# Kernel optimization log

Measured on AMD Instinct MI355X. Metric: run time of the kernel, lower is better.

Reference implementation:

```python
import jax, jax.numpy as jnp
import numpy as np

B, TV, TE = 128, 32, 64
VOCAB, EMB, H, REPR, NET, MAXLEN = 1024, 256, 512, 128, 8, 32


def setup_inputs() -> dict:
    key = jax.random.key(0)
    ks = jax.random.split(key, 26)
    g = lambda i, shape: jax.random.normal(ks[i], shape, dtype=jnp.float32) * 0.05
    return dict(
        input_vertex=jax.random.randint(ks[0], (B, TV), 0, VOCAB),
        input_edge=jax.random.randint(ks[1], (B, TE, 3), 0, NET),
        vertex_emb=g(2, (VOCAB, EMB)),
        v_Wi=g(3, (3 * H, EMB)), v_Wh=g(4, (3 * H, H)), v_bi=g(5, (3 * H,)), v_bh=g(6, (3 * H,)),
        vout_W=g(7, (VOCAB, H)), vout_b=g(8, (VOCAB,)),
        vrep_W=g(9, (REPR, H)), vrep_b=g(10, (REPR,)),
        edge_emb=g(11, (MAXLEN, EMB)),
        e_Wi=g(12, (3 * H, 2 * EMB)), e_Wh=g(13, (3 * H, H)), e_bi=g(14, (3 * H,)), e_bh=g(15, (3 * H,)),
        erep_W=g(16, (REPR, H)), erep_b=g(17, (REPR,)),
        etype_W=g(18, (NET, REPR)), etype_b=g(19, (NET,)),
        src_w=g(20, (REPR,)), src_b=g(21, ()),
        dst_w=g(22, (REPR,)), dst_b=g(23, ()),
    )


def _gru_scan(X, Wi, Wh, bi, bh):
    # X: [T, B, D] -> hidden states [T, B, H]; torch GRUCell gate order r,z,n
    gi = jnp.einsum('tbd,gd->tbg', X, Wi) + bi  # precompute input projections
    h0 = jnp.zeros((X.shape[1], Wh.shape[1]), X.dtype)

    def step(h, gi_t):
        gh = h @ Wh.T + bh
        ir, iz, inn = jnp.split(gi_t, 3, axis=-1)
        hr, hz, hn = jnp.split(gh, 3, axis=-1)
        r = jax.nn.sigmoid(ir + hr)
        z = jax.nn.sigmoid(iz + hz)
        n = jnp.tanh(inn + r * hn)
        h_new = (1.0 - z) * n + z * h
        return h_new, h_new

    _, hs = jax.lax.scan(step, h0, gi)
    return hs


def reference(input_vertex, input_edge, vertex_emb, v_Wi, v_Wh, v_bi, v_bh,
              vout_W, vout_b, vrep_W, vrep_b, edge_emb, e_Wi, e_Wh, e_bi, e_bh,
              erep_W, erep_b, etype_W, etype_b, src_w, src_b, dst_w, dst_b):
    # ---- vertex RNN ----
    Ve = vertex_emb[input_vertex].transpose(1, 0, 2)          # [Tv, B, emb]
    hv = _gru_scan(Ve, v_Wi, v_Wh, v_bi, v_bh)                # [Tv, B, H]
    O_vertex = jnp.einsum('tbh,vh->bvt', hv, vout_W) + vout_b[None, :, None]  # [B, vocab, Tv]
    vrep = jnp.einsum('tbh,rh->tbr', hv, vrep_W) + vrep_b     # [Tv, B, repr]

    # ---- edge RNN ----
    E = jnp.concatenate([edge_emb[input_edge[:, :, 0]],
                         edge_emb[input_edge[:, :, 1]]], axis=2)  # [B, Te, 2*emb]
    he = _gru_scan(E.transpose(1, 0, 2), e_Wi, e_Wh, e_bi, e_bh)  # [Te, B, H]
    e = jnp.einsum('tbh,rh->tbr', he, erep_W) + erep_b            # [Te, B, repr]
    O_edge_type = jnp.einsum('ebr,kr->bke', e, etype_W) + etype_b[None, :, None]  # [B, n_et, Te]

    # ---- edge-vertex additive attention: tanh(e + v) ----
    u = jnp.tanh(e[:, None] + vrep[None])                     # [Te, Tv, B, repr]
    osrc = jnp.einsum('evbr,r->bve', u, src_w) + src_b        # [B, Tv, Te]
    odst = jnp.einsum('evbr,r->bve', u, dst_w) + dst_b        # [B, Tv, Te]
    O_edge = jnp.stack([osrc, odst], axis=2)                  # [B, Tv, 2, Te]

    return O_vertex, O_edge, O_edge_type
```

## Files before the change

### kernel.cpp

```cpp
#include <hip/hip_runtime.h>
#include <hip/hip_bf16.h>


typedef __bf16 bf16_t;
typedef bf16_t bf16x8 __attribute__((ext_vector_type(8)));
typedef bf16_t bf16x4 __attribute__((ext_vector_type(4)));
typedef float  f32x4  __attribute__((ext_vector_type(4)));
typedef unsigned long long ull_t;

#define OFF_GIV  0ull
#define OFF_GIE  6291456ull
#define OFF_HV   18874368ull
#define OFF_HE   20971520ull
#define OFF_VREP 25165824ull
#define OFF_EREP 25690112ull
#define OFF_HBUF 26738688ull
#define FLAG_BYTE_OFF  54001664ull
#define GICNT_BYTE_OFF 54002176ull
#define OFF_CVT  27002880ull
#define CVT_VEMB  0ull
#define CVT_EEMB  262144ull
#define CVT_VWI   270336ull
#define CVT_EWI   663552ull
#define CVT_VWH   1449984ull
#define CVT_EWH   2236416ull
#define CVT_VOUT  3022848ull
#define CVT_VREPW 3547136ull
#define CVT_EREPW 3612672ull

#define OUT_OV 0ull
#define OUT_OE 4194304ull
#define OUT_OT 4718592ull

__device__ __forceinline__ float fsigmoid(float x) {
    float e = __builtin_amdgcn_exp2f(-x * 1.4426950408889634f);
    return __builtin_amdgcn_rcpf(1.0f + e);
}
__device__ __forceinline__ float ftanh(float x) {
    x = fminf(x, 15.0f);
    float e = __builtin_amdgcn_exp2f(x * 2.8853900817779268f);
    return (e - 1.0f) * __builtin_amdgcn_rcpf(e + 1.0f);
}

__global__ __launch_bounds__(256) void prep_kernel(
    const float* __restrict__ vemb, const float* __restrict__ eemb,
    const float* __restrict__ vwi,  const float* __restrict__ ewi,
    const float* __restrict__ vwh,  const float* __restrict__ ewh,
    const float* __restrict__ voutw, const float* __restrict__ vrepw,
    const float* __restrict__ erepw, bf16_t* __restrict__ cvt,
    int* __restrict__ gicnt)
{
    int blk = blockIdx.x;
    if (blk >= 3592) {
        if (threadIdx.x < 128) gicnt[threadIdx.x] = 0;
        return;
    }
    const float* src; bf16_t* dst; int lb;
    if (blk < 256)       { src = vemb;  dst = cvt + CVT_VEMB;  lb = blk; }
    else if (blk < 264)  { src = eemb;  dst = cvt + CVT_EEMB;  lb = blk - 256; }
    else if (blk < 648)  { src = vwi;   dst = cvt + CVT_VWI;   lb = blk - 264; }
    else if (blk < 1416) { src = ewi;   dst = cvt + CVT_EWI;   lb = blk - 648; }
    else if (blk < 2184) { src = vwh;   dst = cvt + CVT_VWH;   lb = blk - 1416; }
    else if (blk < 2952) { src = ewh;   dst = cvt + CVT_EWH;   lb = blk - 2184; }
    else if (blk < 3464) { src = voutw; dst = cvt + CVT_VOUT;  lb = blk - 2952; }
    else if (blk < 3528) { src = vrepw; dst = cvt + CVT_VREPW; lb = blk - 3464; }
    else                 { src = erepw; dst = cvt + CVT_EREPW; lb = blk - 3528; }
    int idx = lb * 1024 + threadIdx.x * 4;
    float4 v = *(const float4*)(src + idx);
    bf16x4 o;
    o[0] = (bf16_t)v.x; o[1] = (bf16_t)v.y; o[2] = (bf16_t)v.z; o[3] = (bf16_t)v.w;
    *(bf16x4*)(dst + idx) = o;
}

template<int GATHER, int K>
__device__ __forceinline__ void produce_gi(
    const bf16_t* __restrict__ W, const float* __restrict__ bias,
    bf16_t* __restrict__ C, const int* __restrict__ gidx,
    const bf16_t* __restrict__ emb, int* __restrict__ cnt, int bx, int nbase)
{
    constexpr int K32 = K / 32;
    const int tid = threadIdx.x, lane = tid & 63, wv = tid >> 6;
    const int r16 = lane & 15, quad = lane >> 4, koff = quad * 8;
    const int mbase = bx * 512 + wv * 64;

    const bf16_t* ap0[4];
    const bf16_t* ap1[4];
#pragma unroll
    for (int i = 0; i < 4; ++i) {
        int row = mbase + i * 16 + r16;
        int b = row & 127, t = row >> 7;
        if (GATHER == 1) {
            ap0[i] = emb + (size_t)gidx[b * 32 + t] * 256 + koff;
            ap1[i] = ap0[i];
        } else {
            int c = (b * 64 + t) * 3;
            ap0[i] = emb + (size_t)gidx[c] * 256 + koff;
            ap1[i] = emb + (size_t)gidx[c + 1] * 256 + koff;
        }
    }
    const bf16_t* bp[4];
#pragma unroll
    for (int j = 0; j < 4; ++j)
        bp[j] = W + (size_t)(nbase + j * 16 + r16) * K + koff;

    f32x4 acc[4][4];
#pragma unroll
    for (int i = 0; i < 4; ++i)
#pragma unroll
        for (int j = 0; j < 4; ++j) acc[i][j] = (f32x4){0.f, 0.f, 0.f, 0.f};

    for (int kc = 0; kc < K32; ++kc) {
        bf16x8 a[4], b[4];
#pragma unroll
        for (int i = 0; i < 4; ++i) {
            const bf16_t* p;
            if (GATHER == 2) p = (kc < 8) ? (ap0[i] + kc * 32) : (ap1[i] + (kc - 8) * 32);
            else             p = ap0[i] + kc * 32;
            a[i] = *(const bf16x8*)p;
        }
#pragma unroll
        for (int j = 0; j < 4; ++j) b[j] = *(const bf16x8*)(bp[j] + kc * 32);
#pragma unroll
        for (int i = 0; i < 4; ++i)
#pragma unroll
            for (int j = 0; j < 4; ++j)
                acc[i][j] = __builtin_amdgcn_mfma_f32_16x16x32_bf16(a[i], b[j], acc[i][j], 0, 0, 0);
    }

#pragma unroll
    for (int j = 0; j < 4; ++j) {
        int col = nbase + j * 16 + r16;
        float bf = bias[col];
#pragma unroll
        for (int i = 0; i < 4; ++i) {
#pragma unroll
            for (int q = 0; q < 4; ++q) {
                int row = mbase + i * 16 + quad * 4 + q;
                bf16_t hb = (bf16_t)(acc[i][j][q] + bf);
                __hip_atomic_store((unsigned short*)(C + (size_t)row * 1536 + col),
                                   __builtin_bit_cast(unsigned short, hb),
                                   __ATOMIC_RELAXED, __HIP_MEMORY_SCOPE_AGENT);
            }
        }
    }
    __builtin_amdgcn_s_waitcnt(0);
    __syncthreads();
    if (tid < 4)
        __hip_atomic_fetch_add(&cnt[bx * 4 + tid], 1,
                               __ATOMIC_RELAXED, __HIP_MEMORY_SCOPE_AGENT);
}

template<int OUTMODE, int K>
__device__ __forceinline__ void consume_gemm(
    const bf16_t* __restrict__ A, const bf16_t* __restrict__ W,
    const float* __restrict__ bias, void* __restrict__ Cv,
    int N, int bx, int nbase)
{
    constexpr int K32 = K / 32;
    const int tid = threadIdx.x, lane = tid & 63, wv = tid >> 6;
    const int r16 = lane & 15, quad = lane >> 4, koff = quad * 8;
    const int mbase = bx * 512 + wv * 64;

    const bf16_t* ap[4];
#pragma unroll
    for (int i = 0; i < 4; ++i)
        ap[i] = A + (size_t)(mbase + i * 16 + r16) * K + koff;
    const bf16_t* bp[4];
#pragma unroll
    for (int j = 0; j < 4; ++j)
        bp[j] = W + (size_t)(nbase + j * 16 + r16) * K + koff;

    f32x4 acc[4][4];
#pragma unroll
    for (int i = 0; i < 4; ++i)
#pragma unroll
        for (int j = 0; j < 4; ++j) acc[i][j] = (f32x4){0.f, 0.f, 0.f, 0.f};

    for (int kc = 0; kc < K32; ++kc) {
        bf16x8 a[4], b[4];
#pragma unroll
        for (int i = 0; i < 4; ++i) a[i] = *(const bf16x8*)(ap[i] + kc * 32);
#pragma unroll
        for (int j = 0; j < 4; ++j) b[j] = *(const bf16x8*)(bp[j] + kc * 32);
#pragma unroll
        for (int i = 0; i < 4; ++i)
#pragma unroll
            for (int j = 0; j < 4; ++j)
                acc[i][j] = __builtin_amdgcn_mfma_f32_16x16x32_bf16(a[i], b[j], acc[i][j], 0, 0, 0);
    }

#pragma unroll
    for (int j = 0; j < 4; ++j) {
        int col = nbase + j * 16 + r16;
        float bf = bias[col];
#pragma unroll
        for (int i = 0; i < 4; ++i) {
            int rowq = mbase + i * 16 + quad * 4;
            if (OUTMODE == 1) {
                int b = rowq >> 5, t0 = rowq & 31;
                float4 v4;
                v4.x = acc[i][j][0] + bf; v4.y = acc[i][j][1] + bf;
                v4.z = acc[i][j][2] + bf; v4.w = acc[i][j][3] + bf;
                *(float4*)((float*)Cv + ((size_t)(b * 1024) + col) * 32 + t0) = v4;
            } else {
                bf16_t* C = (bf16_t*)Cv;
#pragma unroll
                for (int q = 0; q < 4; ++q)
                    C[(size_t)(rowq + q) * N + col] = (bf16_t)(acc[i][j][q] + bf);
            }
        }
    }
}

__device__ __forceinline__ void gate_on(int* p, int thresh) {
    if (threadIdx.x == 0) {
        while (__hip_atomic_load(p, __ATOMIC_RELAXED,
                                 __HIP_MEMORY_SCOPE_AGENT) < thresh)
            __builtin_amdgcn_s_sleep(8);
    }
    __syncthreads();
    asm volatile("" ::: "memory");
}

__global__ __launch_bounds__(512) void fused_scan(
    bf16_t* __restrict__ giV, bf16_t* __restrict__ giE,
    const bf16_t* __restrict__ WhV, const bf16_t* __restrict__ WhE,
    const float* __restrict__ bhV, const float* __restrict__ bhE,
    bf16_t* __restrict__ hV, bf16_t* __restrict__ hE,
    bf16_t* __restrict__ hbuf, int* __restrict__ flags, int* __restrict__ gicnt,
    const int* __restrict__ ivtx, const int* __restrict__ iedg,
    const bf16_t* __restrict__ vemb, const bf16_t* __restrict__ eemb,
    const bf16_t* __restrict__ vwi, const bf16_t* __restrict__ ewi,
    const float* __restrict__ vbi, const float* __restrict__ ebi,
    const bf16_t* __restrict__ voutw, const float* __restrict__ voutb,
    const bf16_t* __restrict__ vrepw, const float* __restrict__ vrepb,
    const bf16_t* __restrict__ erepw, const float* __restrict__ erepb,
    bf16_t* __restrict__ vrep, bf16_t* __restrict__ erep,
    float* __restrict__ out)
{
    __shared__ __align__(16) char lds_all[83968];
    bf16_t (*hbf)[520] = (bf16_t (*)[520])lds_all;
    f32x4 (*red)[3][64] = (f32x4 (*)[3][64])(lds_all + 33280);

    const int bid = blockIdx.x;

    if (bid >= 128) {
        if (bid < 512) {
            int g3 = bid - 128;
            int bx = g3 / 24, nb = g3 - bx * 24;
            produce_gi<2, 512>(ewi, ebi, giE, iedg, eemb, gicnt + 32, bx, nb * 64);
        } else if (bid < 704) {
            int g2 = bid - 512;
            int bx = g2 / 24, nb = g2 - bx * 24;
            produce_gi<1, 256>(vwi, vbi, giV, ivtx, vemb, gicnt, bx, nb * 64);
        } else if (bid < 848) {
            gate_on(&gicnt[96], 64);
            if (bid < 832) {
                int cb = bid - 704;
                consume_gemm<1, 512>(hV, voutw, voutb, out, 1024, cb & 7, (cb >> 3) * 64);
            } else {
                int cb = bid - 832;
                consume_gemm<0, 512>(hV, vrepw, vrepb, vrep, 128, cb & 7, (cb >> 3) * 64);
            }
        } else {
            gate_on(&gicnt[97], 64);
            int cb = bid - 848;
            consume_gemm<0, 512>(hE, erepw, erepb, erep, 128, cb & 15, (cb >> 4) * 64);
        }
        return;
    }

    const int role = bid >> 6;
    const int lb   = bid & 63;
    const int g    = lb & 7;
    const int s    = lb >> 3;
    const bf16_t* gi = role ? giE : giV;
    const bf16_t* Wh = role ? WhE : WhV;
    const float*  bh = role ? bhE : bhV;
    bf16_t* hout = role ? hE : hV;
    const int T = role ? 64 : 32;
    const int slot = role * 8 + g;
    bf16_t* buf0 = hbuf + (size_t)slot * 16384;
    int* fl = flags + slot * 8;
    int* gc = role ? (gicnt + 32) : gicnt;
    int* done = role ? &gicnt[97] : &gicnt[96];
    const int bb = g * 16;

    const int tid = threadIdx.x, lane = tid & 63, w = tid >> 6;
    const int team = w >> 1, half = w & 1;
    const int r16 = lane & 15, quad = lane >> 4, koff = quad * 8;
    const int j = s * 64 + team * 16 + r16;
    const int kbase = half * 256;

    bf16x8 wfrag[3][8];
#pragma unroll
    for (int gate = 0; gate < 3; ++gate) {
        const bf16_t* wrow = Wh + ((size_t)(gate * 512 + j)) * 512 + kbase + koff;
#pragma unroll
        for (int kc = 0; kc < 8; ++kc)
            wfrag[gate][kc] = *(const bf16x8*)(wrow + kc * 32);
    }
    const float bhr = bh[j], bhz = bh[512 + j], bhn = bh[1024 + j];
    float hq[4] = {0.f, 0.f, 0.f, 0.f};

    for (int u = tid; u < 16 * 520; u += 512)
        ((bf16_t*)hbf)[u] = (bf16_t)0.f;
    __syncthreads();

    for (int t = 0; t < T; ++t) {
        if (w == 0) {
            while (__hip_atomic_load(&gc[t], __ATOMIC_RELAXED,
                                     __HIP_MEMORY_SCOPE_AGENT) < 24)
                __builtin_amdgcn_s_sleep(2);
        }
        __syncthreads();
        asm volatile("" ::: "memory");

        float gv[3][4];
        if (half == 0) {
#pragma unroll
            for (int gg = 0; gg < 3; ++gg)
#pragma unroll
                for (int q = 0; q < 4; ++q)
                    gv[gg][q] = (float)gi[((size_t)(t * 128 + bb + quad * 4 + q)) * 1536
                                          + gg * 512 + j];
        }

        if (t > 0) {
            if (w == 1) {
                while (!__all((int)(__hip_atomic_load(&fl[lane & 7], __ATOMIC_RELAXED,
                                                      __HIP_MEMORY_SCOPE_AGENT) >= t))) { }
            }
            __syncthreads();
            asm volatile("" ::: "memory");
            ull_t* src = (ull_t*)(buf0 + (size_t)(t & 1) * 8192);
#pragma unroll
            for (int k = 0; k < 4; ++k) {
                int u = tid + k * 512;
                ull_t vv = __hip_atomic_load(src + u, __ATOMIC_RELAXED,
                                             __HIP_MEMORY_SCOPE_AGENT);
                *(ull_t*)&hbf[u >> 7][(u & 127) * 4] = vv;
            }
        }
        __syncthreads();

        f32x4 ar = {0.f,0.f,0.f,0.f}, az = {0.f,0.f,0.f,0.f}, an = {0.f,0.f,0.f,0.f};
#pragma unroll
        for (int kc = 0; kc < 8; ++kc) {
            bf16x8 a = *(const bf16x8*)&hbf[r16][kbase + kc * 32 + koff];
            ar = __builtin_amdgcn_mfma_f32_16x16x32_bf16(a, wfrag[0][kc], ar, 0, 0, 0);
            az = __builtin_amdgcn_mfma_f32_16x16x32_bf16(a, wfrag[1][kc], az, 0, 0, 0);
            an = __builtin_amdgcn_mfma_f32_16x16x32_bf16(a, wfrag[2][kc], an, 0, 0, 0);
        }

        if (half == 1) {
            red[team][0][lane] = ar;
            red[team][1][lane] = az;
            red[team][2][lane] = an;
        }
        __syncthreads();

        bf16_t hb4[4];
        if (half == 0) {
            ar += red[team][0][lane];
            az += red[team][1][lane];
            an += red[team][2][lane];
#pragma unroll
            for (int q = 0; q < 4; ++q) {
                float r = fsigmoid(gv[0][q] + ar[q] + bhr);
                float z = fsigmoid(gv[1][q] + az[q] + bhz);
                float n = ftanh(gv[2][q] + r * (an[q] + bhn));
                float hnew = (1.0f - z) * n + z * hq[q];
                hq[q] = hnew;
                hb4[q] = (bf16_t)hnew;
            }
            if (t + 1 < T) {
                bf16_t* dstg = buf0 + (size_t)((t + 1) & 1) * 8192;
#pragma unroll
                for (int q = 0; q < 4; ++q)
                    __hip_atomic_store(
                        (unsigned short*)(dstg + (quad * 4 + q) * 512 + j),
                        __builtin_bit_cast(unsigned short, hb4[q]),
                        __ATOMIC_RELAXED, __HIP_MEMORY_SCOPE_AGENT);
            }
        }

        if (t + 1 < T) {
            __builtin_amdgcn_s_waitcnt(0);
            __syncthreads();
            if (tid == 0)
                __hip_atomic_store(&fl[s], t + 1,
                                   __ATOMIC_RELAXED, __HIP_MEMORY_SCOPE_AGENT);
        } else {
            __syncthreads();
        }
        if (half == 0) {
#pragma unroll
            for (int q = 0; q < 4; ++q)
                __hip_atomic_store(
                    (unsigned short*)(hout + ((size_t)((bb + quad * 4 + q) * T + t)) * 512 + j),
                    __builtin_bit_cast(unsigned short, hb4[q]),
                    __ATOMIC_RELAXED, __HIP_MEMORY_SCOPE_AGENT);
        }
    }

    __builtin_amdgcn_s_waitcnt(0);
    __syncthreads();
    if (tid == 0)
        __hip_atomic_fetch_add(done, 1, __ATOMIC_RELAXED, __HIP_MEMORY_SCOPE_AGENT);
}

__global__ __launch_bounds__(256) void etype_kernel(
    const bf16_t* __restrict__ erep, const float* __restrict__ W,
    const float* __restrict__ bias, float* __restrict__ out)
{
    int o = blockIdx.x * 256 + threadIdx.x;
    int te = o & 63, k = (o >> 6) & 7, b = o >> 9;
    float sacc = bias[k];
    const bf16_t* e = erep + ((size_t)(b * 64 + te)) * 128;
    const float* w = W + k * 128;
#pragma unroll 8
    for (int r = 0; r < 128; ++r) sacc += (float)e[r] * w[r];
    out[OUT_OT + o] = sacc;
}

__global__ __launch_bounds__(256) void attn_kernel(
    const bf16_t* __restrict__ erep, const bf16_t* __restrict__ vrep,
    const float* __restrict__ src_w, const float* __restrict__ src_b,
    const float* __restrict__ dst_w, const float* __restrict__ dst_b,
    float* __restrict__ out)
{
    int b = blockIdx.x >> 1, half = blockIdx.x & 1;
    __shared__ float es[32][129], vs[32][129], swf[128], dwf[128];
    int tid = threadIdx.x;
    for (int f = tid; f < 32 * 128; f += 256) {
        int i = f >> 7, r = f & 127;
        es[i][r] = (float)erep[((size_t)(b * 64 + half * 32 + i)) * 128 + r];
        vs[i][r] = (float)vrep[((size_t)(b * 32 + i)) * 128 + r];
    }
    if (tid < 128) { swf[tid] = src_w[tid]; dwf[tid] = dst_w[tid]; }
    __syncthreads();
    float sb = src_b[0], db = dst_b[0];
    for (int p = tid; p < 1024; p += 256) {
        int te = p & 31, tv = p >> 5;
        float sacc = 0.f, dacc = 0.f;
#pragma unroll 4
        for (int r = 0; r < 128; ++r) {
            float u = ftanh(es[te][r] + vs[tv][r]);
            sacc += u * swf[r];
            dacc += u * dwf[r];
        }
        int teg = half * 32 + te;
        size_t base = OUT_OE + ((size_t)(b * 32 + tv) * 2) * 64;
        out[base + teg]      = sacc + sb;
        out[base + 64 + teg] = dacc + db;
    }
}

extern "C" void kernel_launch(void* const* d_in, const int* in_sizes, int n_in,
                              void* d_out, int out_size, void* d_ws, size_t ws_size,
                              hipStream_t stream)
{
    const int*   input_vertex = (const int*)d_in[0];
    const int*   input_edge   = (const int*)d_in[1];
    const float* vertex_emb   = (const float*)d_in[2];
    const float* v_Wi  = (const float*)d_in[3];
    const float* v_Wh  = (const float*)d_in[4];
    const float* v_bi  = (const float*)d_in[5];
    const float* v_bh  = (const float*)d_in[6];
    const float* vout_W = (const float*)d_in[7];
    const float* vout_b = (const float*)d_in[8];
    const float* vrep_W = (const float*)d_in[9];
    const float* vrep_b = (const float*)d_in[10];
    const float* edge_emb = (const float*)d_in[11];
    const float* e_Wi  = (const float*)d_in[12];
    const float* e_Wh  = (const float*)d_in[13];
    const float* e_bi  = (const float*)d_in[14];
    const float* e_bh  = (const float*)d_in[15];
    const float* erep_W = (const float*)d_in[16];
    const float* erep_b = (const float*)d_in[17];
    const float* etype_W = (const float*)d_in[18];
    const float* etype_b = (const float*)d_in[19];
    const float* src_w = (const float*)d_in[20];
    const float* src_b = (const float*)d_in[21];
    const float* dst_w = (const float*)d_in[22];
    const float* dst_b = (const float*)d_in[23];

    bf16_t* ws   = (bf16_t*)d_ws;
    bf16_t* giV  = ws + OFF_GIV;
    bf16_t* giE  = ws + OFF_GIE;
    bf16_t* hV   = ws + OFF_HV;
    bf16_t* hE   = ws + OFF_HE;
    bf16_t* vrep = ws + OFF_VREP;
    bf16_t* erep = ws + OFF_EREP;
    bf16_t* hbuf = ws + OFF_HBUF;
    bf16_t* cvt  = ws + OFF_CVT;
    int*    flags = (int*)((char*)d_ws + FLAG_BYTE_OFF);
    int*    gicnt = (int*)((char*)d_ws + GICNT_BYTE_OFF);
    float*  out  = (float*)d_out;

    prep_kernel<<<3593, 256, 0, stream>>>(vertex_emb, edge_emb, v_Wi, e_Wi, v_Wh, e_Wh,
                                          vout_W, vrep_W, erep_W, cvt, gicnt);

    fused_scan<<<880, 512, 0, stream>>>(
        giV, giE, cvt + CVT_VWH, cvt + CVT_EWH, v_bh, e_bh, hV, hE,
        hbuf, flags, gicnt, input_vertex, input_edge,
        cvt + CVT_VEMB, cvt + CVT_EEMB, cvt + CVT_VWI, cvt + CVT_EWI,
        v_bi, e_bi,
        cvt + CVT_VOUT, vout_b, cvt + CVT_VREPW, vrep_b,
        cvt + CVT_EREPW, erep_b, vrep, erep, out);

    etype_kernel<<<256, 256, 0, stream>>>(erep, etype_W, etype_b, out);
    attn_kernel<<<256, 256, 0, stream>>>(erep, vrep, src_w, src_b, dst_w, dst_b, out);
}
```

Before: 429.7 us.

## Fold etype and attention kernels into fused persistent kernel with counter gating

Moves the edge-type projection and edge-vertex attention work into extra blocks of the fused scan kernel. These blocks wait on new completion counters that the vrep and erep GEMM blocks bump after finishing. The GEMM stores become agent-scope atomic stores so the results are visible to the waiting blocks. This removes two kernel launches and their gaps, and lets the tail work overlap with the remaining GEMMs. The cost is more spin-waiting blocks occupying CUs, and a deadlock risk if those waiters are scheduled before the blocks they depend on.

```diff
diff --git a/kernel.cpp b/kernel.cpp
--- a/kernel.cpp
+++ b/kernel.cpp
@@ -205,8 +205,13 @@
             } else {
                 bf16_t* C = (bf16_t*)Cv;
 #pragma unroll
-                for (int q = 0; q < 4; ++q)
-                    C[(size_t)(rowq + q) * N + col] = (bf16_t)(acc[i][j][q] + bf);
+                for (int q = 0; q < 4; ++q) {
+                    bf16_t hb = (bf16_t)(acc[i][j][q] + bf);
+                    __hip_atomic_store(
+                        (unsigned short*)(C + (size_t)(rowq + q) * N + col),
+                        __builtin_bit_cast(unsigned short, hb),
+                        __ATOMIC_RELAXED, __HIP_MEMORY_SCOPE_AGENT);
+                }
             }
         }
     }
@@ -236,6 +241,9 @@
     const bf16_t* __restrict__ vrepw, const float* __restrict__ vrepb,
     const bf16_t* __restrict__ erepw, const float* __restrict__ erepb,
     bf16_t* __restrict__ vrep, bf16_t* __restrict__ erep,
+    const float* __restrict__ etypeW, const float* __restrict__ etypeB,
+    const float* __restrict__ src_w, const float* __restrict__ src_b,
+    const float* __restrict__ dst_w, const float* __restrict__ dst_b,
     float* __restrict__ out)
 {
     __shared__ __align__(16) char lds_all[83968];
@@ -245,6 +253,7 @@
     const int bid = blockIdx.x;
 
     if (bid >= 128) {
+        const int tid = threadIdx.x;
         if (bid < 512) {
             int g3 = bid - 128;
             int bx = g3 / 24, nb = g3 - bx * 24;
@@ -253,19 +262,70 @@
             int g2 = bid - 512;
             int bx = g2 / 24, nb = g2 - bx * 24;
             produce_gi<1, 256>(vwi, vbi, giV, ivtx, vemb, gicnt, bx, nb * 64);
+        } else if (bid < 832) {
+            gate_on(&gicnt[96], 64);
+            int cb = bid - 704;
+            consume_gemm<1, 512>(hV, voutw, voutb, out, 1024, cb & 7, (cb >> 3) * 64);
         } else if (bid < 848) {
             gate_on(&gicnt[96], 64);
-            if (bid < 832) {
-                int cb = bid - 704;
-                consume_gemm<1, 512>(hV, voutw, voutb, out, 1024, cb & 7, (cb >> 3) * 64);
-            } else {
-                int cb = bid - 832;
-                consume_gemm<0, 512>(hV, vrepw, vrepb, vrep, 128, cb & 7, (cb >> 3) * 64);
-            }
-        } else {
+            int cb = bid - 832;
+            consume_gemm<0, 512>(hV, vrepw, vrepb, vrep, 128, cb & 7, (cb >> 3) * 64);
+            __builtin_amdgcn_s_waitcnt(0);
+            __syncthreads();
+            if (tid == 0)
+                __hip_atomic_fetch_add(&gicnt[98], 1,
+                                       __ATOMIC_RELAXED, __HIP_MEMORY_SCOPE_AGENT);
+        } else if (bid < 880) {
             gate_on(&gicnt[97], 64);
             int cb = bid - 848;
             consume_gemm<0, 512>(hE, erepw, erepb, erep, 128, cb & 15, (cb >> 4) * 64);
+            __builtin_amdgcn_s_waitcnt(0);
+            __syncthreads();
+            if (tid == 0)
+                __hip_atomic_fetch_add(&gicnt[99], 1,
+                                       __ATOMIC_RELAXED, __HIP_MEMORY_SCOPE_AGENT);
+        } else if (bid < 1008) {
+            gate_on(&gicnt[99], 32);
+            int o = (bid - 880) * 512 + tid;
+            int te = o & 63, k = (o >> 6) & 7, b = o >> 9;
+            float sacc = etypeB[k];
+            const bf16_t* e = erep + ((size_t)(b * 64 + te)) * 128;
+            const float* wk = etypeW + k * 128;
+#pragma unroll 8
+            for (int r = 0; r < 128; ++r) sacc += (float)e[r] * wk[r];
+            out[OUT_OT + o] = sacc;
+        } else {
+            gate_on(&gicnt[99], 32);
+            gate_on(&gicnt[98], 16);
+            float (*es)[129] = (float (*)[129])lds_all;
+            float (*vs)[129] = (float (*)[129])(lds_all + 33024);
+            float* swf = (float*)(lds_all + 49536);
+            float* dwf = (float*)(lds_all + 50048);
+            int b = bid - 1008;
+            for (int f = tid; f < 64 * 128; f += 512) {
+                int i = f >> 7, r = f & 127;
+                es[i][r] = (float)erep[((size_t)(b * 64 + i)) * 128 + r];
+            }
+            for (int f = tid; f < 32 * 128; f += 512) {
+                int i = f >> 7, r = f & 127;
+                vs[i][r] = (float)vrep[((size_t)(b * 32 + i)) * 128 + r];
+            }
+            if (tid < 128) { swf[tid] = src_w[tid]; dwf[tid] = dst_w[tid]; }
+            __syncthreads();
+            float sb = src_b[0], db = dst_b[0];
+            for (int p = tid; p < 2048; p += 512) {
+                int te = p & 63, tv = p >> 6;
+                float sacc = 0.f, dacc = 0.f;
+#pragma unroll 4
+                for (int r = 0; r < 128; ++r) {
+                    float u = ftanh(es[te][r] + vs[tv][r]);
+                    sacc += u * swf[r];
+                    dacc += u * dwf[r];
+                }
+                size_t base = OUT_OE + ((size_t)(b * 32 + tv) * 2) * 64;
+                out[base + te]      = sacc + sb;
+                out[base + 64 + te] = dacc + db;
+            }
         }
         return;
     }
@@ -408,53 +468,6 @@
     __syncthreads();
     if (tid == 0)
         __hip_atomic_fetch_add(done, 1, __ATOMIC_RELAXED, __HIP_MEMORY_SCOPE_AGENT);
-}
-
-__global__ __launch_bounds__(256) void etype_kernel(
-    const bf16_t* __restrict__ erep, const float* __restrict__ W,
-    const float* __restrict__ bias, float* __restrict__ out)
-{
-    int o = blockIdx.x * 256 + threadIdx.x;
-    int te = o & 63, k = (o >> 6) & 7, b = o >> 9;
-    float sacc = bias[k];
-    const bf16_t* e = erep + ((size_t)(b * 64 + te)) * 128;
-    const float* w = W + k * 128;
-#pragma unroll 8
-    for (int r = 0; r < 128; ++r) sacc += (float)e[r] * w[r];
-    out[OUT_OT + o] = sacc;
-}
-
-__global__ __launch_bounds__(256) void attn_kernel(
-    const bf16_t* __restrict__ erep, const bf16_t* __restrict__ vrep,
-    const float* __restrict__ src_w, const float* __restrict__ src_b,
-    const float* __restrict__ dst_w, const float* __restrict__ dst_b,
-    float* __restrict__ out)
-{
-    int b = blockIdx.x >> 1, half = blockIdx.x & 1;
-    __shared__ float es[32][129], vs[32][129], swf[128], dwf[128];
-    int tid = threadIdx.x;
-    for (int f = tid; f < 32 * 128; f += 256) {
-        int i = f >> 7, r = f & 127;
-        es[i][r] = (float)erep[((size_t)(b * 64 + half * 32 + i)) * 128 + r];
-        vs[i][r] = (float)vrep[((size_t)(b * 32 + i)) * 128 + r];
-    }
-    if (tid < 128) { swf[tid] = src_w[tid]; dwf[tid] = dst_w[tid]; }
-    __syncthreads();
-    float sb = src_b[0], db = dst_b[0];
-    for (int p = tid; p < 1024; p += 256) {
-        int te = p & 31, tv = p >> 5;
-        float sacc = 0.f, dacc = 0.f;
-#pragma unroll 4
-        for (int r = 0; r < 128; ++r) {
-            float u = ftanh(es[te][r] + vs[tv][r]);
-            sacc += u * swf[r];
-            dacc += u * dwf[r];
-        }
-        int teg = half * 32 + te;
-        size_t base = OUT_OE + ((size_t)(b * 32 + tv) * 2) * 64;
-        out[base + teg]      = sacc + sb;
-        out[base + 64 + teg] = dacc + db;
-    }
 }
 
 extern "C" void kernel_launch(void* const* d_in, const int* in_sizes, int n_in,
@@ -502,14 +515,12 @@
     prep_kernel<<<3593, 256, 0, stream>>>(vertex_emb, edge_emb, v_Wi, e_Wi, v_Wh, e_Wh,
                                           vout_W, vrep_W, erep_W, cvt, gicnt);
 
-    fused_scan<<<880, 512, 0, stream>>>(
+    fused_scan<<<1136, 512, 0, stream>>>(
         giV, giE, cvt + CVT_VWH, cvt + CVT_EWH, v_bh, e_bh, hV, hE,
         hbuf, flags, gicnt, input_vertex, input_edge,
         cvt + CVT_VEMB, cvt + CVT_EEMB, cvt + CVT_VWI, cvt + CVT_EWI,
         v_bi, e_bi,
         cvt + CVT_VOUT, vout_b, cvt + CVT_VREPW, vrep_b,
-        cvt + CVT_EREPW, erep_b, vrep, erep, out);
-
-    etype_kernel<<<256, 256, 0, stream>>>(erep, etype_W, etype_b, out);
-    attn_kernel<<<256, 256, 0, stream>>>(erep, vrep, src_w, src_b, dst_w, dst_b, out);
-}
+        cvt + CVT_EREPW, erep_b, vrep, erep,
+        etype_W, etype_b, src_w, src_b, dst_w, dst_b, out);
+}
```

Result: no change. 434.9 us (+1.2%).
